# Performance work log

Hardware: AMD Instinct MI355X
Metric: run time of the kernel (lower is better)

## Reference

```python
import jax, jax.numpy as jnp
import numpy as np

N = 8192
K = 64
EPS = 1e-7
BN_EPS = 1e-5


def _norm(x):
    return jnp.sqrt(jnp.sum(x * x, axis=-1, keepdims=True))


def _bn(x, gamma, beta):
    # BatchNorm2d in training mode (batch statistics, biased variance)
    mu = jnp.mean(x, axis=(0, 2, 3), keepdims=True)
    var = jnp.mean((x - mu) ** 2, axis=(0, 2, 3), keepdims=True)
    return gamma.reshape(1, -1, 1, 1) * (x - mu) / jnp.sqrt(var + BN_EPS) + beta.reshape(1, -1, 1, 1)


def _conv1x1(x, w, b):
    # 1x1 conv == per-pixel linear: x [B,C,H,W], w [O,C]
    return jnp.einsum('bchw,oc->bohw', x, w) + b.reshape(1, -1, 1, 1)


def setup_inputs() -> dict:
    key = jax.random.key(0)
    ks = jax.random.split(key, 24)
    d = {}
    d['points'] = jax.random.normal(ks[0], (1, N, 3), jnp.float32)
    # graph_conv weights (torch code re-draws these every forward; here fixed params)
    lim0 = float(np.sqrt(6.0 / (4 + 64)))
    d['gw0'] = jax.random.uniform(ks[1], (4, 64), jnp.float32, -lim0, lim0)
    lim = float(np.sqrt(6.0 / (64 + 64)))
    for i in range(1, 5):
        d[f'gw{i}'] = jax.random.uniform(ks[1 + i], (64, 64), jnp.float32, -lim, lim)
    # mlp_1: 4->64->128, mlp_2: 192->256->1024 (1x1 convs + BN)
    d['c1w'] = jax.random.normal(ks[6], (64, 4), jnp.float32) * 0.1
    d['c1b'] = jnp.zeros((64,), jnp.float32)
    d['bn1g'] = jnp.ones((64,), jnp.float32)
    d['bn1b'] = jnp.zeros((64,), jnp.float32)
    d['c2w'] = jax.random.normal(ks[7], (128, 64), jnp.float32) * 0.1
    d['c2b'] = jnp.zeros((128,), jnp.float32)
    d['bn2g'] = jnp.ones((128,), jnp.float32)
    d['bn2b'] = jnp.zeros((128,), jnp.float32)
    d['c3w'] = jax.random.normal(ks[8], (256, 192), jnp.float32) * 0.05
    d['c3b'] = jnp.zeros((256,), jnp.float32)
    d['bn3g'] = jnp.ones((256,), jnp.float32)
    d['bn3b'] = jnp.zeros((256,), jnp.float32)
    d['c4w'] = jax.random.normal(ks[9], (1024, 256), jnp.float32) * 0.05
    d['c4b'] = jnp.zeros((1024,), jnp.float32)
    d['bn4g'] = jnp.ones((1024,), jnp.float32)
    d['bn4b'] = jnp.zeros((1024,), jnp.float32)
    return d


def _knn_search(points, k):
    # pairwise squared distances via ||a||^2 - 2ab + ||b||^2
    r = jnp.sum(points * points, axis=-1, keepdims=True)          # [1,N,1]
    dis = r - 2.0 * jnp.einsum('bnd,bmd->bnm', points, points) + jnp.swapaxes(r, 1, 2)
    _, idx = jax.lax.top_k(-dis, k)                                # [1,N,K]
    knn_pts = jax.vmap(lambda p, i: p[i])(points, idx)             # [1,N,K,3]
    return knn_pts


def _proj_knn(knn_pts):
    b, n, k, _ = knn_pts.shape
    pc = knn_pts - knn_pts[:, :, :1, :]                            # center on first neighbor (self)
    vn = jnp.sqrt(jnp.sum(pc * pc, axis=-1))                       # [1,N,K]
    id1 = jnp.argmax(vn, axis=-1)                                  # farthest neighbor
    a1 = jnp.take_along_axis(pc, jnp.broadcast_to(id1[:, :, None, None], (b, n, 1, 3)), axis=2)[:, :, 0, :]
    a1 = a1 / (_norm(a1) + EPS)
    a2 = jnp.mean(pc, axis=2)
    a2 = a2 / (_norm(a2) + EPS)
    a3 = a1 + 1.5 * a2
    a3 = a3 / (_norm(a3) + EPS)
    den = _norm(pc) + EPS                                          # [1,N,K,1]
    f1 = jnp.sum(pc * a1[:, :, None, :], axis=-1, keepdims=True) / den
    f2 = jnp.sum(pc * a2[:, :, None, :], axis=-1, keepdims=True) / den
    f3 = jnp.sum(pc * a3[:, :, None, :], axis=-1, keepdims=True) / den
    return jnp.concatenate([f1, f2, f3, vn[..., None]], axis=-1)   # [1,N,K,4]


def _proj_points(points):
    b, n, _ = points.shape
    vn = jnp.sqrt(jnp.sum(points * points, axis=-1))               # [1,N]
    i1 = jnp.argmax(vn, axis=-1)
    i2 = jnp.argmin(vn, axis=-1)
    a1 = jnp.take_along_axis(points, jnp.broadcast_to(i1[:, None, None], (b, 1, 3)), axis=1)[:, 0, :]
    a1 = a1 / (_norm(a1) + EPS)
    a2 = jnp.take_along_axis(points, jnp.broadcast_to(i2[:, None, None], (b, 1, 3)), axis=1)[:, 0, :]
    a2 = a2 / (_norm(a2) + EPS)
    a3 = a1 + 1.5 * a2
    a3 = a3 / (_norm(a3) + EPS)
    den = _norm(points) + EPS                                      # [1,N,1]
    f1 = jnp.sum(points * a1[:, None, :], axis=-1, keepdims=True) / den
    f2 = jnp.sum(points * a2[:, None, :], axis=-1, keepdims=True) / den
    f3 = jnp.sum(points * a3[:, None, :], axis=-1, keepdims=True) / den
    return jnp.concatenate([f1, f2, f3, vn[..., None]], axis=-1)   # [1,N,4]


def reference(points, gw0, gw1, gw2, gw3, gw4,
              c1w, c1b, bn1g, bn1b, c2w, c2b, bn2g, bn2b,
              c3w, c3b, bn3g, bn3b, c4w, c4b, bn4g, bn4b):
    n = points.shape[1]
    # upper branch: KNN -> rotation-invariant local feats -> 5-layer MLP -> max over K
    knn_pts = _knn_search(points, K)
    feat_up = _proj_knn(knn_pts)                                   # [1,N,K,4]
    x = feat_up.reshape(-1, 4)
    for w in (gw0, gw1, gw2, gw3, gw4):
        x = jax.nn.relu(x @ w)
    x = x.reshape(1, n, K, 64)
    emb_up = jnp.max(x, axis=2, keepdims=True)                     # [1,N,1,64]
    emb_up = emb_up.reshape(1, 64, n, 1)                           # raw view (reshape), as in torch
    # lower branch: global rotation-invariant feats -> mlp_1
    feat_down = _proj_points(points)                               # [1,N,4]
    emb_down = feat_down.reshape(1, 4, n, 1)                       # raw view (reshape), as in torch
    h = jax.nn.relu(_bn(_conv1x1(emb_down, c1w, c1b), bn1g, bn1b))
    h = jax.nn.relu(_bn(_conv1x1(h, c2w, c2b), bn2g, bn2b))        # [1,128,N,1]
    emb = jnp.concatenate([emb_up, h], axis=1)                     # [1,192,N,1]
    out = jax.nn.relu(_bn(_conv1x1(emb, c3w, c3b), bn3g, bn3b))
    out = jax.nn.relu(_bn(_conv1x1(out, c4w, c4b), bn4g, bn4b))    # [1,1024,N,1]
    return out
```

## Files before the change

kernel.cpp:

```cpp
#include <hip/hip_runtime.h>
#include <hip/hip_bf16.h>

#define NPTS 8192
#define KNN 64
#define EPSF 1e-7f

#define OFF_P4      0
#define OFF_STATS   32768
#define OFF_AVEC    36000
#define OFF_PART    36012
#define OFF_FEATDN  36864
#define OFF_WT1     69632
#define OFF_GWT     69888
#define OFF_BW2     79104
#define OFF_BW3     83200
#define OFF_BW4     107776
#define OFF_XB1     238848
#define OFF_XB3     500992
#define OFF_XB4     1287424
#define OFF_Y1      2336000
#define OFF_Y2      2860288
#define OFF_Y3      3908864
#define OFF_FEATUP  6006016

typedef __bf16 bf16x8 __attribute__((ext_vector_type(8)));
typedef float  f32x4  __attribute__((ext_vector_type(4)));

__device__ __forceinline__ unsigned f2u(float f) {
    unsigned u = __float_as_uint(f);
    return ((int)u >= 0) ? (u | 0x80000000u) : ~u;
}
__device__ __forceinline__ float key_to_f(unsigned long long k) {
    unsigned v = (unsigned)(k >> 32);
    unsigned ob = (v & 0x80000000u) ? (v ^ 0x80000000u) : ~v;
    return __uint_as_float(ob);
}
__device__ __forceinline__ unsigned short f2bf(float x) {
    unsigned u = __float_as_uint(x);
    unsigned r = (u + 0x7FFFu + ((u >> 16) & 1u)) >> 16;
    return (unsigned short)r;
}
__device__ __forceinline__ unsigned long long u64min(unsigned long long a, unsigned long long b){ return a < b ? a : b; }
__device__ __forceinline__ unsigned long long u64max(unsigned long long a, unsigned long long b){ return a < b ? b : a; }

__device__ __forceinline__ unsigned long long sort_merge(
    unsigned long long key, unsigned long long cur, int lane)
{
    #pragma unroll
    for (int k = 2; k <= 64; k <<= 1) {
        #pragma unroll
        for (int j = k >> 1; j > 0; j >>= 1) {
            unsigned long long o = __shfl_xor(key, j);
            bool up = ((lane & k) == 0);
            bool lower = ((lane & j) == 0);
            key = (lower == up) ? u64min(key, o) : u64max(key, o);
        }
    }
    unsigned long long rev = __shfl(key, 63 - lane);
    unsigned long long m = u64min(cur, rev);
    #pragma unroll
    for (int j = 32; j > 0; j >>= 1) {
        unsigned long long o = __shfl_xor(m, j);
        m = ((lane & j) == 0) ? u64min(m, o) : u64max(m, o);
    }
    return m;
}

__global__ __launch_bounds__(256) void prep_a_kernel(
    const float* __restrict__ points, float* __restrict__ ws)
{
    const int n = blockIdx.x * 256 + threadIdx.x;
    float x = points[3*n+0], y = points[3*n+1], z = points[3*n+2];
    float rr = x*x + y*y + z*z;
    ((float4*)(ws + OFF_P4))[n] = make_float4(x, y, z, rr);
    float vn = sqrtf(rr);
    unsigned b = __float_as_uint(vn);
    unsigned long long mxk = ((unsigned long long)b << 32) | (unsigned long long)(0xFFFFFFFFu - (unsigned)n);
    unsigned long long mnk = ((unsigned long long)b << 32) | (unsigned long long)(unsigned)n;
    for (int j = 32; j > 0; j >>= 1) {
        mxk = u64max(mxk, __shfl_xor(mxk, j));
        mnk = u64min(mnk, __shfl_xor(mnk, j));
    }
    __shared__ unsigned long long smx[4], smn[4];
    int wid = threadIdx.x >> 6;
    if ((threadIdx.x & 63) == 0) { smx[wid] = mxk; smn[wid] = mnk; }
    __syncthreads();
    if (threadIdx.x == 0) {
        unsigned long long MX = 0ull, MN = ~0ull;
        for (int i = 0; i < 4; ++i) { MX = u64max(MX, smx[i]); MN = u64min(MN, smn[i]); }
        unsigned long long* parts = (unsigned long long*)(ws + OFF_PART);
        parts[2*blockIdx.x + 0] = MX;
        parts[2*blockIdx.x + 1] = MN;
    }
}

__global__ __launch_bounds__(64) void prep_b_kernel(
    const float* __restrict__ points, float* __restrict__ ws)
{
    const int lane = threadIdx.x;
    const unsigned long long* parts = (const unsigned long long*)(ws + OFF_PART);
    unsigned long long mxk = (lane < 32) ? parts[2*lane + 0] : 0ull;
    unsigned long long mnk = (lane < 32) ? parts[2*lane + 1] : ~0ull;
    for (int j = 32; j > 0; j >>= 1) {
        mxk = u64max(mxk, __shfl_xor(mxk, j));
        mnk = u64min(mnk, __shfl_xor(mnk, j));
    }
    if (lane == 0) {
        int i1 = (int)(0xFFFFFFFFu - (unsigned)(mxk & 0xFFFFFFFFu));
        int i2 = (int)(unsigned)(mnk & 0xFFFFFFFFu);
        float a1x = points[3*i1+0], a1y = points[3*i1+1], a1z = points[3*i1+2];
        float n1 = sqrtf(a1x*a1x + a1y*a1y + a1z*a1z) + EPSF;
        a1x /= n1; a1y /= n1; a1z /= n1;
        float a2x = points[3*i2+0], a2y = points[3*i2+1], a2z = points[3*i2+2];
        float n2 = sqrtf(a2x*a2x + a2y*a2y + a2z*a2z) + EPSF;
        a2x /= n2; a2y /= n2; a2z /= n2;
        float a3x = a1x + 1.5f*a2x, a3y = a1y + 1.5f*a2y, a3z = a1z + 1.5f*a2z;
        float n3 = sqrtf(a3x*a3x + a3y*a3y + a3z*a3z) + EPSF;
        a3x /= n3; a3y /= n3; a3z /= n3;
        float* av = ws + OFF_AVEC;
        av[0]=a1x; av[1]=a1y; av[2]=a1z;
        av[3]=a2x; av[4]=a2y; av[5]=a2z;
        av[6]=a3x; av[7]=a3y; av[8]=a3z;
    }
}

__global__ __launch_bounds__(256) void prep_c_kernel(float* __restrict__ ws)
{
    const int n = blockIdx.x * 256 + threadIdx.x;
    const float* av = ws + OFF_AVEC;
    float4 v = ((const float4*)(ws + OFF_P4))[n];
    float vn = sqrtf(v.w);
    float den = vn + EPSF;
    float f1 = (v.x*av[0] + v.y*av[1] + v.z*av[2]) / den;
    float f2 = (v.x*av[3] + v.y*av[4] + v.z*av[5]) / den;
    float f3 = (v.x*av[6] + v.y*av[7] + v.z*av[8]) / den;
    float4* f4 = (float4*)(ws + OFF_FEATDN + 4*n);
    *f4 = make_float4(f1, f2, f3, vn);
}

__global__ __launch_bounds__(256) void wt_kernel(
    const float* __restrict__ c1w, const float* __restrict__ c2w,
    const float* __restrict__ c3w, const float* __restrict__ c4w,
    const float* __restrict__ gw0, const float* __restrict__ gw1,
    const float* __restrict__ gw2, const float* __restrict__ gw3,
    const float* __restrict__ gw4,
    float* __restrict__ ws)
{
    const int t = blockIdx.x * 256 + threadIdx.x;
    const int T = gridDim.x * 256;
    for (int m = t; m < 2944; m += T) ws[OFF_STATS + m] = 0.f;
    for (int m = t; m < 64*4; m += T) { int o = m >> 2, c = m & 3; ws[OFF_WT1 + c*64 + o] = c1w[m]; }

    unsigned short* bw2 = (unsigned short*)(ws + OFF_BW2);
    for (int m = t; m < 128*64; m += T)   bw2[m] = f2bf(c2w[m]);
    unsigned short* bw3 = (unsigned short*)(ws + OFF_BW3);
    for (int m = t; m < 256*192; m += T)  bw3[m] = f2bf(c3w[m]);
    unsigned short* bw4 = (unsigned short*)(ws + OFF_BW4);
    for (int m = t; m < 1024*256; m += T) bw4[m] = f2bf(c4w[m]);

    unsigned short* gwt = (unsigned short*)(ws + OFF_GWT);
    for (int m = t; m < 2048; m += T) {
        int o = m >> 5, i = m & 31;
        gwt[m] = (i < 4) ? f2bf(gw0[i*64 + o]) : (unsigned short)0;
    }
    const float* gsrc[4] = {gw1, gw2, gw3, gw4};
    for (int l = 0; l < 4; ++l) {
        const float* g = gsrc[l];
        unsigned short* dst = gwt + 2048 + l*4096;
        for (int m = t; m < 4096; m += T) { int o = m >> 6, i = m & 63; dst[m] = f2bf(g[i*64 + o]); }
    }
}

__global__ __launch_bounds__(512) void knn_feat_kernel(
    const float4* __restrict__ p4, float4* __restrict__ feat_up)
{
    __shared__ __align__(16) float4 scand[2048];
    __shared__ unsigned long long queue[8][2][128];
    const int lane = threadIdx.x & 63;
    const int wid  = threadIdx.x >> 6;
    const int q0 = blockIdx.x * 16 + wid * 2;

    const float4 qa = p4[q0];
    const float4 qb = p4[q0 + 1];
    unsigned long long cur0 = ~0ull, cur1 = ~0ull;
    float kthd0 = __builtin_inff(), kthd1 = __builtin_inff();
    int qc0 = 0, qc1 = 0;
    unsigned long long* Q0 = queue[wid][0];
    unsigned long long* Q1 = queue[wid][1];

    for (int base = 0; base < NPTS; base += 2048) {
        __syncthreads();
        for (int t = threadIdx.x; t < 2048; t += 512) scand[t] = p4[base + t];
        __syncthreads();
        #pragma unroll 2
        for (int sub = 0; sub < 2048; sub += 64) {
            float4 cd = scand[sub + lane];
            float dot0 = fmaf(qa.x, cd.x, fmaf(qa.y, cd.y, qa.z * cd.z));
            float d0   = fmaf(-2.f, dot0, qa.w) + cd.w;
            float dot1 = fmaf(qb.x, cd.x, fmaf(qb.y, cd.y, qb.z * cd.z));
            float d1   = fmaf(-2.f, dot1, qb.w) + cd.w;
            bool p0 = d0 < kthd0, p1 = d1 < kthd1;
            unsigned long long m0 = __ballot(p0);
            unsigned long long m1 = __ballot(p1);
            if (m0) {
                int prefix = __builtin_amdgcn_mbcnt_hi((unsigned)(m0 >> 32),
                              __builtin_amdgcn_mbcnt_lo((unsigned)m0, 0));
                if (p0) Q0[qc0 + prefix] = ((unsigned long long)f2u(d0) << 32)
                                         | (unsigned long long)(unsigned)(base + sub + lane);
                qc0 += __popcll(m0);
                if (qc0 >= 64) {
                    qc0 -= 64;
                    cur0 = sort_merge(Q0[qc0 + lane], cur0, lane);
                    kthd0 = key_to_f(__shfl(cur0, 63));
                }
            }
            if (m1) {
                int prefix = __builtin_amdgcn_mbcnt_hi((unsigned)(m1 >> 32),
                              __builtin_amdgcn_mbcnt_lo((unsigned)m1, 0));
                if (p1) Q1[qc1 + prefix] = ((unsigned long long)f2u(d1) << 32)
                                         | (unsigned long long)(unsigned)(base + sub + lane);
                qc1 += __popcll(m1);
                if (qc1 >= 64) {
                    qc1 -= 64;
                    cur1 = sort_merge(Q1[qc1 + lane], cur1, lane);
                    kthd1 = key_to_f(__shfl(cur1, 63));
                }
            }
        }
    }
    cur0 = sort_merge((lane < qc0) ? Q0[lane] : ~0ull, cur0, lane);
    cur1 = sort_merge((lane < qc1) ? Q1[lane] : ~0ull, cur1, lane);

    #pragma unroll 1
    for (int j = 0; j < 2; ++j) {
        unsigned long long cur = j ? cur1 : cur0;
        const int q = q0 + j;
        int nidx = (int)(unsigned)(cur & 0xFFFFFFFFu);
        float4 np = p4[nidx];
        float ox = __shfl(np.x, 0), oy = __shfl(np.y, 0), oz = __shfl(np.z, 0);
        float pcx = np.x - ox, pcy = np.y - oy, pcz = np.z - oz;
        float vn = sqrtf(pcx*pcx + pcy*pcy + pcz*pcz);

        unsigned long long ak = ((unsigned long long)__float_as_uint(vn) << 32)
                              | (unsigned long long)(unsigned)(63 - lane);
        for (int s = 32; s > 0; s >>= 1) ak = u64max(ak, __shfl_xor(ak, s));
        int id1 = 63 - (int)(unsigned)(ak & 0xFFFFFFFFu);

        float a1x = __shfl(pcx, id1), a1y = __shfl(pcy, id1), a1z = __shfl(pcz, id1);
        float n1 = sqrtf(a1x*a1x + a1y*a1y + a1z*a1z) + EPSF;
        a1x /= n1; a1y /= n1; a1z /= n1;

        float sx = pcx, sy = pcy, sz = pcz;
        for (int s = 32; s > 0; s >>= 1) {
            sx += __shfl_xor(sx, s); sy += __shfl_xor(sy, s); sz += __shfl_xor(sz, s);
        }
        float a2x = sx * (1.f/64.f), a2y = sy * (1.f/64.f), a2z = sz * (1.f/64.f);
        float n2 = sqrtf(a2x*a2x + a2y*a2y + a2z*a2z) + EPSF;
        a2x /= n2; a2y /= n2; a2z /= n2;

        float a3x = a1x + 1.5f*a2x, a3y = a1y + 1.5f*a2y, a3z = a1z + 1.5f*a2z;
        float n3 = sqrtf(a3x*a3x + a3y*a3y + a3z*a3z) + EPSF;
        a3x /= n3; a3y /= n3; a3z /= n3;

        float den = vn + EPSF;
        float f1 = (pcx*a1x + pcy*a1y + pcz*a1z) / den;
        float f2 = (pcx*a2x + pcy*a2y + pcz*a2z) / den;
        float f3 = (pcx*a3x + pcy*a3y + pcz*a3z) / den;
        feat_up[q*64 + lane] = make_float4(f1, f2, f3, vn);
    }
}

#define BROW 72
__global__ __launch_bounds__(256) void mlp_kernel(
    const float4* __restrict__ feat_up,
    const unsigned short* __restrict__ gwt,
    unsigned short* __restrict__ xb3)
{
    __shared__ __align__(16) unsigned short Blds[4][64 * BROW];
    const int lane = threadIdx.x & 63;
    const int wid  = threadIdx.x >> 6;
    const int q = blockIdx.x * 4 + wid;
    const int c = lane & 15, g = lane >> 4;
    unsigned short* B = Blds[wid];

    {
        float4 f = feat_up[q*64 + lane];
        uint2 p0;
        p0.x = (unsigned)f2bf(f.x) | ((unsigned)f2bf(f.y) << 16);
        p0.y = (unsigned)f2bf(f.z) | ((unsigned)f2bf(f.w) << 16);
        *(uint2*)&B[lane*BROW] = p0;
        *(uint2*)&B[lane*BROW + 4] = make_uint2(0, 0);
        uint4 z4 = make_uint4(0, 0, 0, 0);
        *(uint4*)&B[lane*BROW + 8]  = z4;
        *(uint4*)&B[lane*BROW + 16] = z4;
        *(uint4*)&B[lane*BROW + 24] = z4;
    }

    const unsigned short* Wl[5] = {gwt, gwt + 2048, gwt + 6144, gwt + 10240, gwt + 14336};
    f32x4 acc[4][4];

    for (int layer = 0; layer < 5; ++layer) {
        const int wstride = (layer == 0) ? 32 : 64;
        const int nks = (layer == 0) ? 1 : 2;
        #pragma unroll
        for (int mb = 0; mb < 4; ++mb)
            #pragma unroll
            for (int nb = 0; nb < 4; ++nb)
                acc[mb][nb] = (f32x4){0.f, 0.f, 0.f, 0.f};

        for (int ks = 0; ks < nks; ++ks) {
            bf16x8 af[4], bf[4];
            #pragma unroll
            for (int mb = 0; mb < 4; ++mb)
                af[mb] = *(const bf16x8*)(Wl[layer] + (mb*16 + c)*wstride + ks*32 + g*8);
            #pragma unroll
            for (int nb = 0; nb < 4; ++nb)
                bf[nb] = *(const bf16x8*)&B[(nb*16 + c)*BROW + ks*32 + g*8];
            #pragma unroll
            for (int mb = 0; mb < 4; ++mb)
                #pragma unroll
                for (int nb = 0; nb < 4; ++nb)
                    acc[mb][nb] = __builtin_amdgcn_mfma_f32_16x16x32_bf16(af[mb], bf[nb], acc[mb][nb], 0, 0, 0);
        }

        if (layer < 4) {
            #pragma unroll
            for (int mb = 0; mb < 4; ++mb) {
                #pragma unroll
                for (int nb = 0; nb < 4; ++nb) {
                    f32x4 a = acc[mb][nb];
                    float r0 = fmaxf(a[0], 0.f), r1 = fmaxf(a[1], 0.f);
                    float r2 = fmaxf(a[2], 0.f), r3 = fmaxf(a[3], 0.f);
                    uint2 pw;
                    pw.x = (unsigned)f2bf(r0) | ((unsigned)f2bf(r1) << 16);
                    pw.y = (unsigned)f2bf(r2) | ((unsigned)f2bf(r3) << 16);
                    *(uint2*)&B[(nb*16 + c)*BROW + mb*16 + g*4] = pw;
                }
            }
        }
    }

    const int cc = q >> 7;
    const int pbase = (q & 127) << 6;
    #pragma unroll
    for (int mb = 0; mb < 4; ++mb) {
        float v[4];
        #pragma unroll
        for (int r = 0; r < 4; ++r)
            v[r] = fmaxf(fmaxf(fmaxf(acc[mb][0][r], acc[mb][1][r]),
                               fmaxf(acc[mb][2][r], acc[mb][3][r])), 0.f);
        #pragma unroll
        for (int mask = 1; mask <= 8; mask <<= 1)
            #pragma unroll
            for (int r = 0; r < 4; ++r)
                v[r] = fmaxf(v[r], __shfl_xor(v[r], mask));
        if (c == 0) {
            #pragma unroll
            for (int r = 0; r < 4; ++r) {
                const int f = mb*16 + g*4 + r;
                xb3[(size_t)(pbase + f) * 192 + cc] = f2bf(v[r]);
            }
        }
    }
}

__global__ __launch_bounds__(256) void conv1_kernel(
    const float* __restrict__ x, const float* __restrict__ wt,
    const float* __restrict__ bias, float* __restrict__ y,
    float* __restrict__ stout)
{
    const int tid = threadIdx.x;
    const int p  = blockIdx.x * 256 + tid;
    const int o0 = blockIdx.y * 32;
    float acc[32];
    #pragma unroll
    for (int u = 0; u < 32; ++u) acc[u] = bias[o0 + u];
    #pragma unroll
    for (int c = 0; c < 4; ++c) {
        float xv = x[c * NPTS + p];
        const float* wr = wt + c * 64 + o0;
        #pragma unroll
        for (int u = 0; u < 32; ++u) acc[u] = fmaf(xv, wr[u], acc[u]);
    }
    #pragma unroll
    for (int u = 0; u < 32; ++u) y[(o0 + u) * NPTS + p] = acc[u];

    __shared__ float ps[4][32], pss[4][32];
    const int wid = tid >> 6, lane = tid & 63;
    #pragma unroll
    for (int u = 0; u < 32; ++u) {
        float s = acc[u], ss = acc[u] * acc[u];
        for (int j = 32; j > 0; j >>= 1) { s += __shfl_xor(s, j); ss += __shfl_xor(ss, j); }
        if (lane == 0) { ps[wid][u] = s; pss[wid][u] = ss; }
    }
    __syncthreads();
    if (tid < 32) {
        float S  = ps[0][tid] + ps[1][tid] + ps[2][tid] + ps[3][tid];
        float SS = pss[0][tid] + pss[1][tid] + pss[2][tid] + pss[3][tid];
        atomicAdd(&stout[o0 + tid], S);
        atomicAdd(&stout[64 + o0 + tid], SS);
    }
}

__global__ __launch_bounds__(256) void bnpack_kernel(
    const float* __restrict__ y, const float* __restrict__ st,
    const float* __restrict__ gam, const float* __restrict__ bet,
    int C, int stride, int coff, unsigned short* __restrict__ xb)
{
    __shared__ float sc[256], sh[256];
    __shared__ __align__(16) unsigned short tile[64][264];
    const int tid = threadIdx.x;
    for (int cc = tid; cc < C; cc += 256) {
        float mu  = st[cc] * (1.f / 8192.f);
        float var = st[C + cc] * (1.f / 8192.f) - mu * mu;
        float s = gam[cc] / sqrtf(var + 1e-5f);
        sc[cc] = s; sh[cc] = bet[cc] - mu * s;
    }
    __syncthreads();
    const int pl = tid & 63, g = tid >> 6;
    const int p = blockIdx.x * 64 + pl;
    for (int c0 = g * 8; c0 < C; c0 += 32) {
        unsigned pk[4];
        #pragma unroll
        for (int h = 0; h < 4; ++h) {
            float v0 = fmaxf(fmaf(y[(c0 + 2*h    ) * NPTS + p], sc[c0 + 2*h    ], sh[c0 + 2*h    ]), 0.f);
            float v1 = fmaxf(fmaf(y[(c0 + 2*h + 1) * NPTS + p], sc[c0 + 2*h + 1], sh[c0 + 2*h + 1]), 0.f);
            pk[h] = (unsigned)f2bf(v0) | ((unsigned)f2bf(v1) << 16);
        }
        *(uint4*)&tile[pl][c0] = make_uint4(pk[0], pk[1], pk[2], pk[3]);
    }
    __syncthreads();
    const int cpr = C >> 3;
    const int nch = 64 * cpr;
    for (int idx = tid; idx < nch; idx += 256) {
        int r = idx / cpr, cc = (idx - r * cpr) * 8;
        *(uint4*)&xb[(size_t)(blockIdx.x * 64 + r) * stride + coff + cc] = *(uint4*)&tile[r][cc];
    }
}

__global__ __launch_bounds__(256) void conv_mfma_kernel(
    const unsigned short* __restrict__ A, const unsigned short* __restrict__ Bx,
    const float* __restrict__ bias, int K, int M,
    float* __restrict__ y, float* __restrict__ stout)
{
    const int lane = threadIdx.x & 63;
    const int w = threadIdx.x >> 6;
    const int n0 = blockIdx.x * 256 + w * 64;
    const int m0 = blockIdx.y * 64;
    const int c = lane & 15, g = lane >> 4;

    f32x4 acc[4][4];
    #pragma unroll
    for (int mt = 0; mt < 4; ++mt)
        #pragma unroll
        for (int nt = 0; nt < 4; ++nt)
            acc[mt][nt] = (f32x4){0.f, 0.f, 0.f, 0.f};

    for (int k0 = 0; k0 < K; k0 += 32) {
        bf16x8 af[4], bf[4];
        #pragma unroll
        for (int mt = 0; mt < 4; ++mt)
            af[mt] = *(const bf16x8*)(A + (size_t)(m0 + mt*16 + c) * K + k0 + g*8);
        #pragma unroll
        for (int nt = 0; nt < 4; ++nt)
            bf[nt] = *(const bf16x8*)(Bx + (size_t)(n0 + nt*16 + c) * K + k0 + g*8);
        #pragma unroll
        for (int mt = 0; mt < 4; ++mt)
            #pragma unroll
            for (int nt = 0; nt < 4; ++nt)
                acc[mt][nt] = __builtin_amdgcn_mfma_f32_16x16x32_bf16(af[mt], bf[nt], acc[mt][nt], 0, 0, 0);
    }

    #pragma unroll
    for (int mt = 0; mt < 4; ++mt) {
        float s[4], ss[4];
        #pragma unroll
        for (int r = 0; r < 4; ++r) {
            const int o = m0 + mt*16 + g*4 + r;
            const float bv = bias[o];
            float sum = 0.f, sq = 0.f;
            #pragma unroll
            for (int nt = 0; nt < 4; ++nt) {
                float v = acc[mt][nt][r] + bv;
                y[(size_t)o * NPTS + n0 + nt*16 + c] = v;
                sum += v; sq += v * v;
            }
            s[r] = sum; ss[r] = sq;
        }
        #pragma unroll
        for (int mask = 1; mask <= 8; mask <<= 1)
            #pragma unroll
            for (int r = 0; r < 4; ++r) {
                s[r]  += __shfl_xor(s[r],  mask);
                ss[r] += __shfl_xor(ss[r], mask);
            }
        if (c == 0) {
            #pragma unroll
            for (int r = 0; r < 4; ++r) {
                const int o = m0 + mt*16 + g*4 + r;
                atomicAdd(&stout[o], s[r]);
                atomicAdd(&stout[M + o], ss[r]);
            }
        }
    }
}

__global__ __launch_bounds__(256) void bnrelu_kernel(
    const float* y, const float* __restrict__ st,
    const float* __restrict__ g, const float* __restrict__ b,
    float* out, int C)
{
    int idx = blockIdx.x * 256 + threadIdx.x;
    int c = idx >> 13;
    float mu  = st[c] * (1.f / 8192.f);
    float var = st[C + c] * (1.f / 8192.f) - mu * mu;
    float scale = g[c] / sqrtf(var + 1e-5f);
    float v = fmaf(y[idx] - mu, scale, b[c]);
    out[idx] = fmaxf(v, 0.f);
}

extern "C" void kernel_launch(void* const* d_in, const int* in_sizes, int n_in,
                              void* d_out, int out_size, void* d_ws, size_t ws_size,
                              hipStream_t stream) {
    const float* points = (const float*)d_in[0];
    const float* gw0 = (const float*)d_in[1];
    const float* gw1 = (const float*)d_in[2];
    const float* gw2 = (const float*)d_in[3];
    const float* gw3 = (const float*)d_in[4];
    const float* gw4 = (const float*)d_in[5];
    const float* c1w = (const float*)d_in[6];  const float* c1b = (const float*)d_in[7];
    const float* bn1g = (const float*)d_in[8]; const float* bn1b = (const float*)d_in[9];
    const float* c2w = (const float*)d_in[10]; const float* c2b = (const float*)d_in[11];
    const float* bn2g = (const float*)d_in[12];const float* bn2b = (const float*)d_in[13];
    const float* c3w = (const float*)d_in[14]; const float* c3b = (const float*)d_in[15];
    const float* bn3g = (const float*)d_in[16];const float* bn3b = (const float*)d_in[17];
    const float* c4w = (const float*)d_in[18]; const float* c4b = (const float*)d_in[19];
    const float* bn4g = (const float*)d_in[20];const float* bn4b = (const float*)d_in[21];

    float* ws = (float*)d_ws;
    float* p4f    = ws + OFF_P4;
    float* featdn = ws + OFF_FEATDN;
    float* featup = ws + OFF_FEATUP;
    float* y1 = ws + OFF_Y1; float* y2 = ws + OFF_Y2; float* y3 = ws + OFF_Y3;
    float* s1 = ws + OFF_STATS + 0;
    float* s2 = ws + OFF_STATS + 128;
    float* s3 = ws + OFF_STATS + 384;
    float* s4 = ws + OFF_STATS + 896;
    float* wt1 = ws + OFF_WT1;
    const unsigned short* gwt = (const unsigned short*)(ws + OFF_GWT);
    const unsigned short* bw2 = (const unsigned short*)(ws + OFF_BW2);
    const unsigned short* bw3 = (const unsigned short*)(ws + OFF_BW3);
    const unsigned short* bw4 = (const unsigned short*)(ws + OFF_BW4);
    unsigned short* xb1 = (unsigned short*)(ws + OFF_XB1);
    unsigned short* xb3 = (unsigned short*)(ws + OFF_XB3);
    unsigned short* xb4 = (unsigned short*)(ws + OFF_XB4);
    float* outp = (float*)d_out;

    prep_a_kernel<<<32, 256, 0, stream>>>(points, ws);
    prep_b_kernel<<<1, 64, 0, stream>>>(points, ws);
    prep_c_kernel<<<32, 256, 0, stream>>>(ws);
    wt_kernel<<<256, 256, 0, stream>>>(c1w, c2w, c3w, c4w, gw0, gw1, gw2, gw3, gw4, ws);

    knn_feat_kernel<<<512, 512, 0, stream>>>((const float4*)p4f, (float4*)featup);
    mlp_kernel<<<2048, 256, 0, stream>>>((const float4*)featup, gwt, xb3);

    conv1_kernel<<<dim3(32, 2), 256, 0, stream>>>(featdn, wt1, c1b, y1, s1);
    bnpack_kernel<<<128, 256, 0, stream>>>(y1, s1, bn1g, bn1b, 64, 64, 0, xb1);
    conv_mfma_kernel<<<dim3(32, 2), 256, 0, stream>>>(bw2, xb1, c2b, 64, 128, y2, s2);
    bnpack_kernel<<<128, 256, 0, stream>>>(y2, s2, bn2g, bn2b, 128, 192, 64, xb3);
    conv_mfma_kernel<<<dim3(32, 4), 256, 0, stream>>>(bw3, xb3, c3b, 192, 256, y3, s3);
    bnpack_kernel<<<128, 256, 0, stream>>>(y3, s3, bn3g, bn3b, 256, 256, 0, xb4);
    conv_mfma_kernel<<<dim3(32, 16), 256, 0, stream>>>(bw4, xb4, c4b, 256, 1024, outp, s4);
    bnrelu_kernel<<<1024*32, 256, 0, stream>>>(outp, s4, bn4g, bn4b, outp, 1024);
}
```

Measured before the change: 370.8 us.

## Prune KNN search with x-binned spatial sort and bounding-box early exit

Points are bucketed by x coordinate into 64 bins through a counting sort (atomic histogram, prefix sum, scatter), and per-64-point tile x bounds are computed. Each wave of queries then grows outward from its own tile and stops once the x-gap to the next tile exceeds the current k-th distance for both queries, so most of the brute-force all-pairs scan is skipped. The cost is several extra small kernels and atomics, plus candidate loads from global memory instead of an LDS-staged tile. Tie ordering among equal distances may differ from the full scan because candidates are visited in a different order.

```diff
diff --git a/kernel.cpp b/kernel.cpp
--- a/kernel.cpp
+++ b/kernel.cpp
@@ -23,6 +23,13 @@
 #define OFF_Y3      3908864
 #define OFF_FEATUP  6006016
 
+#define OFF_P4S     OFF_Y1
+#define OFF_SIDX    (OFF_Y1 + 32768)
+#define OFF_TBND    (OFF_Y1 + 40960)
+#define OFF_BCNT    (OFF_Y1 + 41216)
+#define OFF_BOFS    (OFF_Y1 + 41280)
+#define OFF_BFIL    (OFF_Y1 + 41348)
+
 typedef __bf16 bf16x8 __attribute__((ext_vector_type(8)));
 typedef float  f32x4  __attribute__((ext_vector_type(4)));
 
@@ -66,6 +73,11 @@
     return m;
 }
 
+__device__ __forceinline__ int xbin(float x) {
+    int b = (int)((x + 4.5f) * (64.0f / 9.0f));
+    return min(63, max(0, b));
+}
+
 __global__ __launch_bounds__(256) void prep_a_kernel(
     const float* __restrict__ points, float* __restrict__ ws)
 {
@@ -73,6 +85,7 @@
     float x = points[3*n+0], y = points[3*n+1], z = points[3*n+2];
     float rr = x*x + y*y + z*z;
     ((float4*)(ws + OFF_P4))[n] = make_float4(x, y, z, rr);
+    atomicAdd((int*)(ws + OFF_BCNT) + xbin(x), 1);
     float vn = sqrtf(rr);
     unsigned b = __float_as_uint(vn);
     unsigned long long mxk = ((unsigned long long)b << 32) | (unsigned long long)(0xFFFFFFFFu - (unsigned)n);
@@ -122,6 +135,14 @@
         av[3]=a2x; av[4]=a2y; av[5]=a2z;
         av[6]=a3x; av[7]=a3y; av[8]=a3z;
     }
+    if (lane == 1) {
+        const int* cnt = (const int*)(ws + OFF_BCNT);
+        int* ofs = (int*)(ws + OFF_BOFS);
+        int* fil = (int*)(ws + OFF_BFIL);
+        int acc = 0;
+        for (int i = 0; i < 64; ++i) { ofs[i] = acc; fil[i] = acc; acc += cnt[i]; }
+        ofs[64] = acc;
+    }
 }
 
 __global__ __launch_bounds__(256) void prep_c_kernel(float* __restrict__ ws)
@@ -138,6 +159,27 @@
     *f4 = make_float4(f1, f2, f3, vn);
 }
 
+__global__ __launch_bounds__(256) void scatter_kernel(float* __restrict__ ws)
+{
+    const int n = blockIdx.x * 256 + threadIdx.x;
+    float4 v = ((const float4*)(ws + OFF_P4))[n];
+    int pos = atomicAdd((int*)(ws + OFF_BFIL) + xbin(v.x), 1);
+    ((float4*)(ws + OFF_P4S))[pos] = v;
+    ((int*)(ws + OFF_SIDX))[pos] = n;
+}
+
+__global__ __launch_bounds__(64) void bounds_kernel(float* __restrict__ ws)
+{
+    const int t = blockIdx.x, lane = threadIdx.x;
+    float x = ((const float4*)(ws + OFF_P4S))[t*64 + lane].x;
+    float mn = x, mx = x;
+    for (int j = 32; j > 0; j >>= 1) {
+        mn = fminf(mn, __shfl_xor(mn, j));
+        mx = fmaxf(mx, __shfl_xor(mx, j));
+    }
+    if (lane == 0) { ws[OFF_TBND + 2*t] = mn; ws[OFF_TBND + 2*t + 1] = mx; }
+}
+
 __global__ __launch_bounds__(256) void wt_kernel(
     const float* __restrict__ c1w, const float* __restrict__ c2w,
     const float* __restrict__ c3w, const float* __restrict__ c4w,
@@ -149,6 +191,7 @@
     const int t = blockIdx.x * 256 + threadIdx.x;
     const int T = gridDim.x * 256;
     for (int m = t; m < 2944; m += T) ws[OFF_STATS + m] = 0.f;
+    for (int m = t; m < 64; m += T) ((int*)(ws + OFF_BCNT))[m] = 0;
     for (int m = t; m < 64*4; m += T) { int o = m >> 2, c = m & 3; ws[OFF_WT1 + c*64 + o] = c1w[m]; }
 
     unsigned short* bw2 = (unsigned short*)(ws + OFF_BW2);
@@ -172,61 +215,83 @@
 }
 
 __global__ __launch_bounds__(512) void knn_feat_kernel(
-    const float4* __restrict__ p4, float4* __restrict__ feat_up)
-{
-    __shared__ __align__(16) float4 scand[2048];
+    const float4* __restrict__ p4,
+    const float4* __restrict__ p4s,
+    const int*    __restrict__ sidx,
+    const float*  __restrict__ tbnd,
+    float4* __restrict__ feat_up)
+{
+    __shared__ float sb[256];
     __shared__ unsigned long long queue[8][2][128];
     const int lane = threadIdx.x & 63;
     const int wid  = threadIdx.x >> 6;
-    const int q0 = blockIdx.x * 16 + wid * 2;
-
-    const float4 qa = p4[q0];
-    const float4 qb = p4[q0 + 1];
+    for (int i = threadIdx.x; i < 256; i += 512) sb[i] = tbnd[i];
+    __syncthreads();
+
+    const int s0 = blockIdx.x * 16 + wid * 2;
+    const float4 qa = p4s[s0];
+    const float4 qb = p4s[s0 + 1];
+    const int qi0 = sidx[s0], qi1 = sidx[s0 + 1];
     unsigned long long cur0 = ~0ull, cur1 = ~0ull;
     float kthd0 = __builtin_inff(), kthd1 = __builtin_inff();
     int qc0 = 0, qc1 = 0;
     unsigned long long* Q0 = queue[wid][0];
     unsigned long long* Q1 = queue[wid][1];
 
-    for (int base = 0; base < NPTS; base += 2048) {
-        __syncthreads();
-        for (int t = threadIdx.x; t < 2048; t += 512) scand[t] = p4[base + t];
-        __syncthreads();
-        #pragma unroll 2
-        for (int sub = 0; sub < 2048; sub += 64) {
-            float4 cd = scand[sub + lane];
-            float dot0 = fmaf(qa.x, cd.x, fmaf(qa.y, cd.y, qa.z * cd.z));
-            float d0   = fmaf(-2.f, dot0, qa.w) + cd.w;
-            float dot1 = fmaf(qb.x, cd.x, fmaf(qb.y, cd.y, qb.z * cd.z));
-            float d1   = fmaf(-2.f, dot1, qb.w) + cd.w;
-            bool p0 = d0 < kthd0, p1 = d1 < kthd1;
-            unsigned long long m0 = __ballot(p0);
-            unsigned long long m1 = __ballot(p1);
-            if (m0) {
-                int prefix = __builtin_amdgcn_mbcnt_hi((unsigned)(m0 >> 32),
-                              __builtin_amdgcn_mbcnt_lo((unsigned)m0, 0));
-                if (p0) Q0[qc0 + prefix] = ((unsigned long long)f2u(d0) << 32)
-                                         | (unsigned long long)(unsigned)(base + sub + lane);
-                qc0 += __popcll(m0);
-                if (qc0 >= 64) {
-                    qc0 -= 64;
-                    cur0 = sort_merge(Q0[qc0 + lane], cur0, lane);
-                    kthd0 = key_to_f(__shfl(cur0, 63));
-                }
+    int L = s0 >> 6, R = s0 >> 6;
+    int t = L;
+    for (;;) {
+        float4 cd = p4s[t*64 + lane];
+        int ci = sidx[t*64 + lane];
+        float dot0 = fmaf(qa.x, cd.x, fmaf(qa.y, cd.y, qa.z * cd.z));
+        float d0   = fmaf(-2.f, dot0, qa.w) + cd.w;
+        float dot1 = fmaf(qb.x, cd.x, fmaf(qb.y, cd.y, qb.z * cd.z));
+        float d1   = fmaf(-2.f, dot1, qb.w) + cd.w;
+        bool p0 = d0 < kthd0, p1 = d1 < kthd1;
+        unsigned long long m0 = __ballot(p0);
+        unsigned long long m1 = __ballot(p1);
+        if (m0) {
+            int prefix = __builtin_amdgcn_mbcnt_hi((unsigned)(m0 >> 32),
+                          __builtin_amdgcn_mbcnt_lo((unsigned)m0, 0));
+            if (p0) Q0[qc0 + prefix] = ((unsigned long long)f2u(d0) << 32)
+                                     | (unsigned long long)(unsigned)ci;
+            qc0 += __popcll(m0);
+            if (qc0 >= 64) {
+                qc0 -= 64;
+                cur0 = sort_merge(Q0[qc0 + lane], cur0, lane);
+                kthd0 = key_to_f(__shfl(cur0, 63));
             }
-            if (m1) {
-                int prefix = __builtin_amdgcn_mbcnt_hi((unsigned)(m1 >> 32),
-                              __builtin_amdgcn_mbcnt_lo((unsigned)m1, 0));
-                if (p1) Q1[qc1 + prefix] = ((unsigned long long)f2u(d1) << 32)
-                                         | (unsigned long long)(unsigned)(base + sub + lane);
-                qc1 += __popcll(m1);
-                if (qc1 >= 64) {
-                    qc1 -= 64;
-                    cur1 = sort_merge(Q1[qc1 + lane], cur1, lane);
-                    kthd1 = key_to_f(__shfl(cur1, 63));
-                }
+        }
+        if (m1) {
+            int prefix = __builtin_amdgcn_mbcnt_hi((unsigned)(m1 >> 32),
+                          __builtin_amdgcn_mbcnt_lo((unsigned)m1, 0));
+            if (p1) Q1[qc1 + prefix] = ((unsigned long long)f2u(d1) << 32)
+                                     | (unsigned long long)(unsigned)ci;
+            qc1 += __popcll(m1);
+            if (qc1 >= 64) {
+                qc1 -= 64;
+                cur1 = sort_merge(Q1[qc1 + lane], cur1, lane);
+                kthd1 = key_to_f(__shfl(cur1, 63));
             }
         }
+        bool canL = false, canR = false;
+        float gapL = 0.f, gapR = 0.f;
+        if (L > 0) {
+            float mx = sb[2*(L-1) + 1];
+            float g0 = qa.x - mx, g1 = qb.x - mx;
+            bool e0 = (g0 > 0.f) && (g0*g0 >= kthd0);
+            bool e1 = (g1 > 0.f) && (g1*g1 >= kthd1);
+            if (!(e0 && e1)) { canL = true; gapL = fminf(fmaxf(g0, 0.f), fmaxf(g1, 0.f)); }
+        }
+        if (R < 127) {
+            float mn = sb[2*(R+1)];
+            float g0 = mn - qa.x, g1 = mn - qb.x;
+            bool e0 = (g0 > 0.f) && (g0*g0 >= kthd0);
+            bool e1 = (g1 > 0.f) && (g1*g1 >= kthd1);
+            if (!(e0 && e1)) { canR = true; gapR = fminf(fmaxf(g0, 0.f), fmaxf(g1, 0.f)); }
+        }
+        if (!canL && !canR) break;
+        t = (canL && (!canR || gapL <= gapR)) ? --L : ++R;
     }
     cur0 = sort_merge((lane < qc0) ? Q0[lane] : ~0ull, cur0, lane);
     cur1 = sort_merge((lane < qc1) ? Q1[lane] : ~0ull, cur1, lane);
@@ -234,7 +299,7 @@
     #pragma unroll 1
     for (int j = 0; j < 2; ++j) {
         unsigned long long cur = j ? cur1 : cur0;
-        const int q = q0 + j;
+        const int q = j ? qi1 : qi0;
         int nidx = (int)(unsigned)(cur & 0xFFFFFFFFu);
         float4 np = p4[nidx];
         float ox = __shfl(np.x, 0), oy = __shfl(np.y, 0), oz = __shfl(np.z, 0);
@@ -556,12 +621,16 @@
     unsigned short* xb4 = (unsigned short*)(ws + OFF_XB4);
     float* outp = (float*)d_out;
 
+    wt_kernel<<<256, 256, 0, stream>>>(c1w, c2w, c3w, c4w, gw0, gw1, gw2, gw3, gw4, ws);
     prep_a_kernel<<<32, 256, 0, stream>>>(points, ws);
     prep_b_kernel<<<1, 64, 0, stream>>>(points, ws);
     prep_c_kernel<<<32, 256, 0, stream>>>(ws);
-    wt_kernel<<<256, 256, 0, stream>>>(c1w, c2w, c3w, c4w, gw0, gw1, gw2, gw3, gw4, ws);
-
-    knn_feat_kernel<<<512, 512, 0, stream>>>((const float4*)p4f, (float4*)featup);
+    scatter_kernel<<<32, 256, 0, stream>>>(ws);
+    bounds_kernel<<<128, 64, 0, stream>>>(ws);
+
+    knn_feat_kernel<<<512, 512, 0, stream>>>(
+        (const float4*)(ws + OFF_P4), (const float4*)(ws + OFF_P4S),
+        (const int*)(ws + OFF_SIDX), ws + OFF_TBND, (float4*)featup);
     mlp_kernel<<<2048, 256, 0, stream>>>((const float4*)featup, gwt, xb3);
 
     conv1_kernel<<<dim3(32, 2), 256, 0, stream>>>(featdn, wt1, c1b, y1, s1);
```

Result: slower. 416.2 us (+12.3%).
